# Kernel tuning notes

Measured on AMD Instinct MI355X. Metric: run time of the kernel, lower is better.

## Reference

```python
import jax, jax.numpy as jnp
import numpy as np

NUM_HEADS = 8


def setup_inputs() -> dict:
    key = jax.random.key(0)
    ks = jax.random.split(key, 7)
    B, C, L = 4, 512, 2048
    s = 1.0 / np.sqrt(C)
    return {
        "x": jax.random.normal(ks[0], (B, C, L), dtype=jnp.float32),
        "wq": jax.random.normal(ks[1], (C, C), dtype=jnp.float32) * s,
        "bq": jax.random.normal(ks[2], (C,), dtype=jnp.float32) * 0.01,
        "wk": jax.random.normal(ks[3], (C, C), dtype=jnp.float32) * s,
        "bk": jax.random.normal(ks[4], (C,), dtype=jnp.float32) * 0.01,
        "wv": jax.random.normal(ks[5], (C, C), dtype=jnp.float32) * s,
        "bv": jax.random.normal(ks[6], (C,), dtype=jnp.float32) * 0.01,
    }


def reference(x, wq, bq, wk, bk, wv, bv):
    B, C, L = x.shape
    H = NUM_HEADS
    Ch = C // H

    def proj(w, b):
        # 1x1 Conv1d == per-position channel GEMM: (B,C,L) x (O,C) -> (B,O,L)
        return jnp.einsum('bcl,oc->bol', x, w) + b[None, :, None]

    q = proj(wq, bq).reshape(B, H, Ch, L)
    k = proj(wk, bk).reshape(B, H, Ch, L)
    v = proj(wv, bv).reshape(B, H, Ch, L)

    # q^T k over channel dim -> (B,H,L,L)
    scale = 1.0 / jnp.sqrt(jnp.asarray(Ch, dtype=x.dtype))
    scores = jnp.einsum('bhcl,bhcm->bhlm', q, k) * scale
    attn = jax.nn.softmax(scores, axis=-1)

    # FAITHFUL quirk: torch code uses .view (reshape), NOT transpose, on v
    v2 = v.reshape(B, H, L, Ch)
    out = jnp.einsum('bhlm,bhmc->bhlc', attn, v2)
    # and .view back to (B, C, L) — again a plain reshape
    return out.reshape(B, C, L)
```

## Files before the change

kernel.cpp:

```cpp
#include <hip/hip_runtime.h>


typedef unsigned short u16;
typedef unsigned int   u32;
typedef short bf16x8 __attribute__((ext_vector_type(8)));
typedef u16  u16x8  __attribute__((ext_vector_type(8)));
typedef float f32x16 __attribute__((ext_vector_type(16)));

#define SCALE_Q 0.18033688011112042f

__device__ __forceinline__ u16 f2b(float f) {
    u32 u = __float_as_uint(f);
    u += 0x7FFFu + ((u >> 16) & 1u);
    return (u16)(u >> 16);
}

__device__ __forceinline__ float exp2_(float x) {
#if __has_builtin(__builtin_amdgcn_exp2f)
    return __builtin_amdgcn_exp2f(x);
#else
    return exp2f(x);
#endif
}

__device__ __forceinline__ u32 cvtpk(float lo, float hi) {
    u32 d;
    asm("v_cvt_pk_bf16_f32 %0, %1, %2" : "=v"(d) : "v"(lo), "v"(hi));
    return d;
}

__device__ __forceinline__ void pl32swap(u32& a, u32& b) {
    asm volatile("v_permlane32_swap_b32 %0, %1" : "+v"(a), "+v"(b));
}

__device__ __forceinline__ void g2l16(const u16* g, u16* l) {
    __builtin_amdgcn_global_load_lds(
        (const __attribute__((address_space(1))) unsigned int*)g,
        (__attribute__((address_space(3))) unsigned int*)l, 16, 0, 0);
}

#define WAITV(N) asm volatile("s_waitcnt vmcnt(" #N ")" ::: "memory")
#define WAITL0   asm volatile("s_waitcnt lgkmcnt(0)" ::: "memory")
#define SBAR     __builtin_amdgcn_s_barrier()
#define SCHED0   __builtin_amdgcn_sched_barrier(0)

__global__ __launch_bounds__(256) void prep_kernel(
    const float* __restrict__ wq, const float* __restrict__ wk,
    const float* __restrict__ wv, const float* __restrict__ x,
    u16* __restrict__ wcat, u16* __restrict__ xT)
{
    const int bid = blockIdx.x, t = threadIdx.x;
    if (bid < 384) {
        int e0 = bid * 2048 + t * 8;
        const float* src = (e0 < 262144) ? wq : (e0 < 524288) ? wk : wv;
        int eo = e0 & 262143;
        float4 a = *(const float4*)(src + eo);
        float4 b = *(const float4*)(src + eo + 4);
        u16x8 o;
        o[0]=f2b(a.x); o[1]=f2b(a.y); o[2]=f2b(a.z); o[3]=f2b(a.w);
        o[4]=f2b(b.x); o[5]=f2b(b.y); o[6]=f2b(b.z); o[7]=f2b(b.w);
        *(u16x8*)(wcat + e0) = o;
        return;
    }
    int xb = bid - 384;
    int b = xb >> 8, ct = (xb >> 5) & 7, lt = xb & 31;
    __shared__ float lds[64 * 65];
#pragma unroll
    for (int it = 0; it < 4; ++it) {
        int s = t + it * 256;
        int cr = s >> 4, l4 = (s & 15) * 4;
        float4 v = *(const float4*)(x + ((size_t)(b * 512 + ct * 64 + cr)) * 2048 + lt * 64 + l4);
        lds[(l4 + 0) * 65 + cr] = v.x;
        lds[(l4 + 1) * 65 + cr] = v.y;
        lds[(l4 + 2) * 65 + cr] = v.z;
        lds[(l4 + 3) * 65 + cr] = v.w;
    }
    __syncthreads();
    {
        int l = t >> 2, c16 = (t & 3) * 16;
        u16x8 o0, o1;
#pragma unroll
        for (int i = 0; i < 8; ++i) o0[i] = f2b(lds[l * 65 + c16 + i]);
#pragma unroll
        for (int i = 0; i < 8; ++i) o1[i] = f2b(lds[l * 65 + c16 + 8 + i]);
        u16* d = xT + ((size_t)(b * 2048 + lt * 64 + l)) * 512 + ct * 64 + c16;
        *(u16x8*)d = o0;
        *(u16x8*)(d + 8) = o1;
    }
}

__global__ __launch_bounds__(256) void proj_kernel(
    const u16* __restrict__ wcat, const u16* __restrict__ xT,
    const float* __restrict__ bq, const float* __restrict__ bk,
    const float* __restrict__ bv,
    u16* __restrict__ qt, u16* __restrict__ kt, u16* __restrict__ vv)
{
    const int lt = blockIdx.x, ot = blockIdx.y, b = blockIdx.z;
    const int l0 = lt * 128, o0 = ot * 128;
    const int sel = o0 >> 9, ol0 = o0 & 511;
    const float* __restrict__ bias = (sel == 0) ? bq : (sel == 1) ? bk : bv;

    __shared__ __align__(16) u16 wt[128 * 64];
    __shared__ __align__(16) u16 xt[128 * 64];

    const int tid = threadIdx.x, wid = tid >> 6, lane = tid & 63;
    const int hlf = lane >> 5, i32 = lane & 31;
    const int lrow = lane >> 3, lg = lane & 7;
    const int wo = wid >> 1, wl = wid & 1;

    f32x16 acc[2][2];
#pragma unroll
    for (int a = 0; a < 2; ++a)
#pragma unroll
        for (int c = 0; c < 2; ++c)
#pragma unroll
            for (int r = 0; r < 16; ++r) acc[a][c][r] = 0.f;

    for (int c0 = 0; c0 < 512; c0 += 64) {
#pragma unroll
        for (int cc = 0; cc < 4; ++cc) {
            int rb = (wid * 4 + cc) * 8;
            int rw = rb + lrow;
            int sg = (lg ^ (rw & 7)) << 3;
            g2l16(wcat + (size_t)(o0 + rw) * 512 + c0 + sg, wt + rb * 64);
            g2l16(xT + ((size_t)(b * 2048 + l0 + rw)) * 512 + c0 + sg, xt + rb * 64);
        }
        WAITV(0);
        SBAR;
        SCHED0;
        bf16x8 wf[2][4], xf[2][4];
#pragma unroll
        for (int a = 0; a < 2; ++a)
#pragma unroll
            for (int ks = 0; ks < 4; ++ks) {
                int rw = wo * 64 + a * 32 + i32;
                wf[a][ks] = *(const bf16x8*)(wt + rw * 64 + (((ks * 2 + hlf) ^ (rw & 7)) << 3));
                int rx = wl * 64 + a * 32 + i32;
                xf[a][ks] = *(const bf16x8*)(xt + rx * 64 + (((ks * 2 + hlf) ^ (rx & 7)) << 3));
            }
        if (sel < 2) {
#pragma unroll
            for (int a = 0; a < 2; ++a)
#pragma unroll
                for (int c = 0; c < 2; ++c)
#pragma unroll
                    for (int ks = 0; ks < 4; ++ks)
                        acc[a][c] = __builtin_amdgcn_mfma_f32_32x32x16_bf16(xf[a][ks], wf[c][ks], acc[a][c], 0, 0, 0);
        } else {
#pragma unroll
            for (int a = 0; a < 2; ++a)
#pragma unroll
                for (int c = 0; c < 2; ++c)
#pragma unroll
                    for (int ks = 0; ks < 4; ++ks)
                        acc[a][c] = __builtin_amdgcn_mfma_f32_32x32x16_bf16(wf[a][ks], xf[c][ks], acc[a][c], 0, 0, 0);
        }
        WAITL0;
        SCHED0;
        SBAR;
    }

    if (sel < 2) {
        u16* __restrict__ dst = (sel == 0) ? qt : kt;
        const float sc = (sel == 0) ? SCALE_Q : 1.0f;
#pragma unroll
        for (int c = 0; c < 2; ++c) {
            int cg = ol0 + wo * 64 + c * 32 + i32;
            int h = cg >> 6, c6 = cg & 63;
            float bb = bias[cg];
#pragma unroll
            for (int a = 0; a < 2; ++a)
#pragma unroll
                for (int r = 0; r < 16; ++r) {
                    int l = l0 + wl * 64 + a * 32 + (r & 3) + 8 * (r >> 2) + 4 * hlf;
                    dst[(((size_t)(b * 8 + h)) * 2048 + l) * 64 + c6] = f2b((acc[a][c][r] + bb) * sc);
                }
        }
    } else {
#pragma unroll
        for (int a = 0; a < 2; ++a)
#pragma unroll
            for (int r = 0; r < 16; ++r) {
                int ov = ol0 + wo * 64 + a * 32 + (r & 3) + 8 * (r >> 2) + 4 * hlf;
                float bb = bias[ov];
#pragma unroll
                for (int c = 0; c < 2; ++c) {
                    int l = l0 + wl * 64 + c * 32 + i32;
                    vv[((size_t)(b * 512 + ov)) * 2048 + l] = f2b(acc[a][c][r] + bb);
                }
            }
    }
}

__global__ __launch_bounds__(256) void vtrans_kernel(
    const u16* __restrict__ vv, u16* __restrict__ vtg)
{
    const int bh = blockIdx.x >> 5, mt = blockIdx.x & 31;
    const u16* __restrict__ src = vv + (size_t)bh * 131072 + mt * 4096;
    __shared__ u16 lds[64 * 65];
    const int t = threadIdx.x;
    const int m = t >> 2, c16 = (t & 3) * 16;
    u16x8 a = *(const u16x8*)(src + t * 16);
    u16x8 b = *(const u16x8*)(src + t * 16 + 8);
#pragma unroll
    for (int i = 0; i < 8; ++i) lds[(c16 + i) * 65 + m] = a[i];
#pragma unroll
    for (int i = 0; i < 8; ++i) lds[(c16 + 8 + i) * 65 + m] = b[i];
    __syncthreads();
    const int c = t >> 2, m16 = (t & 3) * 16;
    u16x8 o0, o1;
#pragma unroll
    for (int i = 0; i < 8; ++i) o0[i] = lds[c * 65 + m16 + i];
#pragma unroll
    for (int i = 0; i < 8; ++i) o1[i] = lds[c * 65 + m16 + 8 + i];
    u16* d = vtg + (size_t)bh * 131072 + (size_t)c * 2048 + mt * 64 + m16;
    *(u16x8*)d = o0;
    *(u16x8*)(d + 8) = o1;
}

__global__ __launch_bounds__(128) void attn_kernel(
    const u16* __restrict__ qt, const u16* __restrict__ kt,
    const u16* __restrict__ vtg, float* __restrict__ out)
{
    const int bh = blockIdx.y;
    const int l0 = blockIdx.x * 64;
    const int tid = threadIdx.x, wid = tid >> 6, lane = tid & 63;
    const int hlf = lane >> 5, i32 = lane & 31;
    const int lrow = lane >> 3, lg = lane & 7;

    __shared__ __align__(16) u16 smem[16384];
    float* olds = (float*)smem;

    bf16x8 qf[4];
    {
        const u16* qrow = qt + ((size_t)bh * 2048 + l0 + wid * 32 + i32) * 64;
#pragma unroll
        for (int ks = 0; ks < 4; ++ks)
            qf[ks] = *(const bf16x8*)(qrow + ks * 16 + hlf * 8);
    }
    const u16* __restrict__ kb = kt + (size_t)bh * 2048 * 64;
    const u16* __restrict__ vb = vtg + (size_t)bh * 131072;

    float m_run = -1e30f, l_run = 0.f;
    f32x16 oacc[2];
#pragma unroll
    for (int c = 0; c < 2; ++c)
#pragma unroll
        for (int r = 0; r < 16; ++r) oacc[c][r] = 0.f;

#define STAGE(T, BUF) do {                                                        \
    if (wid == 0) {                                                               \
        _Pragma("unroll")                                                         \
        for (int cc = 0; cc < 8; ++cc) {                                          \
            int mrow = (T) * 64 + cc * 8 + lrow;                                  \
            g2l16(kb + (size_t)mrow * 64 + ((lg ^ lrow) << 3),                    \
                  smem + (BUF) * 4096 + cc * 512);                                \
        }                                                                         \
    } else {                                                                      \
        _Pragma("unroll")                                                         \
        for (int cc = 0; cc < 8; ++cc) {                                          \
            int crow = cc * 8 + lrow;                                             \
            g2l16(vb + (size_t)crow * 2048 + (T) * 64 + ((lg ^ lrow) << 3),       \
                  smem + 8192 + (BUF) * 4096 + cc * 512);                         \
        }                                                                         \
    } } while (0)

    STAGE(0, 0);

    for (int t = 0; t < 32; ++t) {
        const int cb = t & 1;
        if (t < 31) {
            STAGE(t + 1, cb ^ 1);
            WAITV(8);
        } else {
            WAITV(0);
        }
        SBAR;
        SCHED0;

        const u16* kbuf = smem + cb * 4096;
        const u16* vbuf = smem + 8192 + cb * 4096;

        f32x16 st[2];
#pragma unroll
        for (int mi = 0; mi < 2; ++mi) {
#pragma unroll
            for (int r = 0; r < 16; ++r) st[mi][r] = 0.f;
#pragma unroll
            for (int ks = 0; ks < 4; ++ks) {
                int row = mi * 32 + i32;
                bf16x8 kf = *(const bf16x8*)(kbuf + row * 64 + (((ks * 2 + hlf) ^ (row & 7)) << 3));
                st[mi] = __builtin_amdgcn_mfma_f32_32x32x16_bf16(kf, qf[ks], st[mi], 0, 0, 0);
            }
        }

        float pmax = st[0][0];
#pragma unroll
        for (int mi = 0; mi < 2; ++mi)
#pragma unroll
            for (int r = 0; r < 16; ++r) pmax = fmaxf(pmax, st[mi][r]);
        pmax = fmaxf(pmax, __shfl_xor(pmax, 32));
        float m_new = fmaxf(m_run, pmax);
        float corr = exp2_(m_run - m_new);
        float psum = 0.f;
#pragma unroll
        for (int mi = 0; mi < 2; ++mi)
#pragma unroll
            for (int r = 0; r < 16; ++r) {
                st[mi][r] = exp2_(st[mi][r] - m_new);
                psum += st[mi][r];
            }
        psum += __shfl_xor(psum, 32);
        l_run = l_run * corr + psum;
        m_run = m_new;
#pragma unroll
        for (int c = 0; c < 2; ++c)
#pragma unroll
            for (int r = 0; r < 16; ++r) oacc[c][r] *= corr;

        bf16x8 pf[4];
#pragma unroll
        for (int ks = 0; ks < 4; ++ks) {
            int mi = ks >> 1, rb = (ks & 1) * 8;
            u32 A1 = cvtpk(st[mi][rb + 0], st[mi][rb + 1]);
            u32 B1 = cvtpk(st[mi][rb + 2], st[mi][rb + 3]);
            u32 A2 = cvtpk(st[mi][rb + 4], st[mi][rb + 5]);
            u32 B2 = cvtpk(st[mi][rb + 6], st[mi][rb + 7]);
            pl32swap(A1, A2);
            pl32swap(B1, B2);
            union { u32 w[4]; bf16x8 v; } u;
            u.w[0] = A1; u.w[1] = B1; u.w[2] = A2; u.w[3] = B2;
            pf[ks] = u.v;
        }

#pragma unroll
        for (int ci = 0; ci < 2; ++ci)
#pragma unroll
            for (int ks = 0; ks < 4; ++ks) {
                int row = ci * 32 + i32;
                bf16x8 vf = *(const bf16x8*)(vbuf + row * 64 + (((ks * 2 + hlf) ^ (row & 7)) << 3));
                oacc[ci] = __builtin_amdgcn_mfma_f32_32x32x16_bf16(vf, pf[ks], oacc[ci], 0, 0, 0);
            }

        WAITL0;
        SCHED0;
        SBAR;
    }

    float inv = 1.0f / l_run;
    int ll = wid * 32 + i32;
#pragma unroll
    for (int ci = 0; ci < 2; ++ci)
#pragma unroll
        for (int r = 0; r < 16; ++r) {
            int c = ci * 32 + (r & 3) + 8 * (r >> 2) + 4 * hlf;
            olds[ll * 64 + (c ^ ((ll & 7) << 2))] = oacc[ci][r] * inv;
        }
    __syncthreads();
    {
        int l = tid >> 1, hv = tid & 1;
        float* orow = out + ((size_t)bh * 2048 + l0 + l) * 64;
#pragma unroll
        for (int i = 0; i < 8; ++i) {
            int c4 = hv * 8 + i;
            float4 v = *(const float4*)(olds + l * 64 + ((c4 ^ (l & 7)) << 2));
            *(float4*)(orow + c4 * 4) = v;
        }
    }
#undef STAGE
}

extern "C" void kernel_launch(void* const* d_in, const int* in_sizes, int n_in,
                              void* d_out, int out_size, void* d_ws, size_t ws_size,
                              hipStream_t stream) {
    const float* x  = (const float*)d_in[0];
    const float* wq = (const float*)d_in[1];
    const float* bq = (const float*)d_in[2];
    const float* wk = (const float*)d_in[3];
    const float* bk = (const float*)d_in[4];
    const float* wv = (const float*)d_in[5];
    const float* bv = (const float*)d_in[6];
    float* out = (float*)d_out;

    u16* wcat = (u16*)d_ws;
    u16* xT   = wcat + 786432;
    u16* qt   = xT + 4194304;
    u16* kt   = qt + 4194304;
    u16* vv   = kt + 4194304;
    u16* vtg  = vv + 4194304;

    prep_kernel<<<1408, 256, 0, stream>>>(wq, wk, wv, x, wcat, xT);
    proj_kernel<<<dim3(16, 12, 4), 256, 0, stream>>>(wcat, xT, bq, bk, bv, qt, kt, vv);
    vtrans_kernel<<<1024, 256, 0, stream>>>(vv, vtg);
    attn_kernel<<<dim3(32, 32), 128, 0, stream>>>(qt, kt, vtg, out);
}
```

Before: 111.8 us.

## Split attention KV loop across two blocks and merge with combine kernel

Splits the key/value sequence into two halves handled by separate blocks (grid z=2), in the style of flash-decoding. Each half writes unnormalized partial outputs plus its running max and sum into recycled workspace buffers. A new combine kernel rescales and merges the two partials. This doubles the block count from 1024 to 2048 so more of the GPU is occupied, at the cost of extra global traffic for the partials and an additional kernel launch.

After: 127.2 us. +13.8%, slower.

```diff
diff --git a/kernel.cpp b/kernel.cpp
--- a/kernel.cpp
+++ b/kernel.cpp
@@ -220,10 +220,14 @@
 
 __global__ __launch_bounds__(128) void attn_kernel(
     const u16* __restrict__ qt, const u16* __restrict__ kt,
-    const u16* __restrict__ vtg, float* __restrict__ out)
+    const u16* __restrict__ vtg, float* __restrict__ out,
+    float* __restrict__ p1a, float* __restrict__ p1b,
+    float* __restrict__ ls0, float* __restrict__ ls1,
+    float* __restrict__ ms0, float* __restrict__ ms1)
 {
     const int bh = blockIdx.y;
     const int l0 = blockIdx.x * 64;
+    const int mh = blockIdx.z;
     const int tid = threadIdx.x, wid = tid >> 6, lane = tid & 63;
     const int hlf = lane >> 5, i32 = lane & 31;
     const int lrow = lane >> 3, lg = lane & 7;
@@ -265,12 +269,13 @@
         }                                                                         \
     } } while (0)
 
-    STAGE(0, 0);
-
-    for (int t = 0; t < 32; ++t) {
+    const int t0 = mh * 16;
+    STAGE(t0, 0);
+
+    for (int t = 0; t < 16; ++t) {
         const int cb = t & 1;
-        if (t < 31) {
-            STAGE(t + 1, cb ^ 1);
+        if (t < 15) {
+            STAGE(t0 + t + 1, cb ^ 1);
             WAITV(8);
         } else {
             WAITV(0);
@@ -347,19 +352,27 @@
         SBAR;
     }
 
-    float inv = 1.0f / l_run;
+    if (lane < 32) {
+        size_t ridx = (size_t)bh * 2048 + l0 + wid * 32 + lane;
+        ((mh == 0) ? ls0 : ls1)[ridx] = l_run;
+        ((mh == 0) ? ms0 : ms1)[ridx] = m_run;
+    }
+
+    float* dstbase = (mh == 0)
+        ? (out + (size_t)bh * 131072)
+        : (((bh < 16) ? p1a : p1b) + (size_t)(bh & 15) * 131072);
     int ll = wid * 32 + i32;
 #pragma unroll
     for (int ci = 0; ci < 2; ++ci)
 #pragma unroll
         for (int r = 0; r < 16; ++r) {
             int c = ci * 32 + (r & 3) + 8 * (r >> 2) + 4 * hlf;
-            olds[ll * 64 + (c ^ ((ll & 7) << 2))] = oacc[ci][r] * inv;
+            olds[ll * 64 + (c ^ ((ll & 7) << 2))] = oacc[ci][r];
         }
     __syncthreads();
     {
         int l = tid >> 1, hv = tid & 1;
-        float* orow = out + ((size_t)bh * 2048 + l0 + l) * 64;
+        float* orow = dstbase + (size_t)(l0 + l) * 64;
 #pragma unroll
         for (int i = 0; i < 8; ++i) {
             int c4 = hv * 8 + i;
@@ -368,6 +381,31 @@
         }
     }
 #undef STAGE
+}
+
+__global__ __launch_bounds__(256) void combine_kernel(
+    float* __restrict__ out,
+    const float* __restrict__ p1a, const float* __restrict__ p1b,
+    const float* __restrict__ ls0, const float* __restrict__ ls1,
+    const float* __restrict__ ms0, const float* __restrict__ ms1)
+{
+    int q = blockIdx.x * 256 + threadIdx.x;
+    int e = q * 4;
+    int row = e >> 6;
+    int bh = e >> 17;
+    float m0 = ms0[row], m1 = ms1[row];
+    float M = fmaxf(m0, m1);
+    float w0 = exp2_(m0 - M), w1 = exp2_(m1 - M);
+    float inv = 1.0f / (ls0[row] * w0 + ls1[row] * w1);
+    float4 a = *(const float4*)(out + e);
+    const float* psrc = (bh < 16) ? p1a : p1b;
+    float4 b = *(const float4*)(psrc + (e & 2097151));
+    float4 r;
+    r.x = (a.x * w0 + b.x * w1) * inv;
+    r.y = (a.y * w0 + b.y * w1) * inv;
+    r.z = (a.z * w0 + b.z * w1) * inv;
+    r.w = (a.w * w0 + b.w * w1) * inv;
+    *(float4*)(out + e) = r;
 }
 
 extern "C" void kernel_launch(void* const* d_in, const int* in_sizes, int n_in,
@@ -389,8 +427,17 @@
     u16* vv   = kt + 4194304;
     u16* vtg  = vv + 4194304;
 
+    float* ls0 = (float*)wcat;
+    float* ls1 = ls0 + 65536;
+    float* ms0 = ls1 + 65536;
+    float* ms1 = ms0 + 65536;
+    float* p1a = (float*)xT;
+    float* p1b = (float*)vv;
+
     prep_kernel<<<1408, 256, 0, stream>>>(wq, wk, wv, x, wcat, xT);
     proj_kernel<<<dim3(16, 12, 4), 256, 0, stream>>>(wcat, xT, bq, bk, bv, qt, kt, vv);
     vtrans_kernel<<<1024, 256, 0, stream>>>(vv, vtg);
-    attn_kernel<<<dim3(32, 32), 128, 0, stream>>>(qt, kt, vtg, out);
-}
+    attn_kernel<<<dim3(32, 32, 2), 128, 0, stream>>>(qt, kt, vtg, out, p1a, p1b,
+                                                     ls0, ls1, ms0, ms1);
+    combine_kernel<<<4096, 256, 0, stream>>>(out, p1a, p1b, ls0, ls1, ms0, ms1);
+}
```
